# Optimization experiments

Hardware: AMD Instinct MI355X
Metric: run time of the kernel (lower is better)

## Reference

```python
import jax, jax.numpy as jnp
import numpy as np

B, I, D, H, DP = 2, 256, 768, 12, 128
DK = D // H  # 64
NPQ, NPV = 4, 8  # query/key points and value points per head


def setup_inputs() -> dict:
    key = jax.random.key(0)
    ks = jax.random.split(key, 24)
    s = 0.02
    w = lambda k, shp: (jax.random.normal(k, shp, jnp.float32) * s)
    inp = {
        "x1d": jax.random.normal(ks[0], (B, I, D), jnp.float32),
        "x2d": jax.random.normal(ks[1], (B, I, I, DP), jnp.float32),
        "past_T": jax.random.normal(ks[2], (B, I, 3), jnp.float32),
        "past_R": jax.random.normal(ks[3], (B, I, 3, 3), jnp.float32),
        "last_T": jax.random.normal(ks[4], (B, I, 3), jnp.float32),
        "last_R": jax.random.normal(ks[5], (B, I, 3, 3), jnp.float32),
        "bias": jax.random.normal(ks[6], (B, H, I, I), jnp.float32) * 0.1,
        "Wq": w(ks[7], (D, D)),
        "Wk": w(ks[8], (D, D)),
        "Wv": w(ks[9], (D, D)),
        "W_pair_bias": w(ks[10], (DP, H)),
        "Wpq_past": w(ks[11], (D, H * NPQ * 3)),
        "Wpk_past": w(ks[12], (D, H * NPQ * 3)),
        "Wpv_past": w(ks[13], (D, H * NPV * 3)),
        "Wpq_last": w(ks[14], (D, H * NPQ * 3)),
        "Wpk_last": w(ks[15], (D, H * NPQ * 3)),
        "Wpv_last": w(ks[16], (D, H * NPV * 3)),
        "tpw_past": jax.random.uniform(ks[17], (H,), jnp.float32),
        "tpw_last": jax.random.uniform(ks[18], (H,), jnp.float32),
        "W_pair_value": w(ks[19], (DP, D)),
        "W_out": w(ks[20], (2 * D + 2 * H * 8 * 4, D)),
        "b_out": jnp.zeros((D,), jnp.float32),
    }
    return inp


def reference(x1d, x2d, past_T, past_R, last_T, last_R, bias,
              Wq, Wk, Wv, W_pair_bias,
              Wpq_past, Wpk_past, Wpv_past,
              Wpq_last, Wpk_last, Wpv_last,
              tpw_past, tpw_last, W_pair_value, W_out, b_out):
    b, i, d = x1d.shape
    h = tpw_past.shape[0]
    dk = d // h
    scalar_w = 1.0 / np.sqrt(3.0 * dk)
    point_w = 1.0 / np.sqrt(3.0 * 4.0 * 9.0 / 2.0)
    pair_w = 1.0 / np.sqrt(3.0)

    # scalar attention
    q = (x1d @ Wq).reshape(b, i, h, dk)
    k = (x1d @ Wk).reshape(b, i, h, dk)
    v = (x1d @ Wv).reshape(b, i, h, dk)
    scalar_attn = jnp.einsum('bihc,bjhc->bhij', q * scalar_w, k)

    past_IR = jnp.swapaxes(past_R, -1, -2)
    last_IR = jnp.swapaxes(last_R, -1, -2)

    def affine(pts, T, IR):  # pts: [b,i,h,c,3]
        return jnp.einsum('bipq,bihcq->bihcp', IR, pts) + T[:, :, None, None, :]

    def point_branch(Wpq, Wpk, Wpv, T, IR, tpw):
        qp = (x1d @ Wpq).reshape(b, i, h, NPQ, 3)
        kp = (x1d @ Wpk).reshape(b, i, h, NPQ, 3)
        vp = (x1d @ Wpv).reshape(b, i, h, NPV, 3)
        qg, kg, vg = affine(qp, T, IR), affine(kp, T, IR), affine(vp, T, IR)
        # pairwise point distances: [b,i,j,h,NPQ]
        dist = jnp.linalg.norm(qg[:, :, None] - kg[:, None], axis=-1)
        pw = point_w * jax.nn.softplus(tpw)  # [h]
        attn = -0.5 * pw[:, None, None] * jnp.transpose(dist.sum(-1), (0, 3, 1, 2))
        return attn, vg

    pa_past, vg_past = point_branch(Wpq_past, Wpk_past, Wpv_past, past_T, past_IR, tpw_past)
    pa_last, vg_last = point_branch(Wpq_last, Wpk_last, Wpv_last, last_T, last_IR, tpw_last)

    pair_attn = pair_w * jnp.transpose(x2d @ W_pair_bias, (0, 3, 1, 2))  # bhij

    attn = jax.nn.softmax(scalar_attn + pa_past + pa_last + pair_attn + bias, axis=-1)

    out_scalar = jnp.einsum('bhij,bjhc->bihc', attn, v).reshape(b, i, d)
    og_past = jnp.einsum('bhij,bjhcp->bihcp', attn, vg_past)
    og_last = jnp.einsum('bhij,bjhcp->bihcp', attn, vg_last)

    # NOTE: the original module inverts BOTH branches with the PAST pose (faithful).
    def inv_past(og):
        return jnp.einsum('bipq,bihcq->bihcp', past_R, og - past_T[:, :, None, None, :])

    ol_past = inv_past(og_past)
    ol_last = inv_past(og_last)
    n_past = jnp.linalg.norm(ol_past, axis=-1).reshape(b, i, h * NPV)
    n_last = jnp.linalg.norm(ol_last, axis=-1).reshape(b, i, h * NPV)
    ol_past = ol_past.reshape(b, i, h * NPV * 3)
    ol_last = ol_last.reshape(b, i, h * NPV * 3)

    v_pair = (x2d @ W_pair_value).reshape(b, i, i, h, dk)
    out_pair = jnp.einsum('bhij,bijhc->bihc', attn, v_pair).reshape(b, i, d)

    feat = jnp.concatenate([out_pair, out_scalar, ol_past, n_past, ol_last, n_last], axis=-1)
    return feat @ W_out + b_out  # dropout is identity at eval
```

## Files before the change

kernel.cpp:

```cpp
#include <hip/hip_runtime.h>
#include <hip/hip_bf16.h>
#include <math.h>

#define BB 2
#define II 256
#define DD 768
#define HH 12
#define DPP 128
#define NPQ 4
#define NPV 8
#define FEAT_DIM 2304
#define NPACK 3456

#define OFF_QKVPTS ((size_t)0)
#define OFF_PBATTN ((size_t)1769472)
#define OFF_X1DB   ((size_t)3342336)
#define OFF_VT     OFF_X1DB
#define OFF_W1T    ((size_t)3538944)
#define OFF_ABF    OFF_W1T
#define OFF_W2T    ((size_t)4866048)
#define OFF_FEATB  ((size_t)5750784)
#define OFF_QPTS   ((size_t)6340608)
#define OFF_KPTS   ((size_t)6488064)
#define OFF_QKHM   ((size_t)6635520)
#define OFF_VGJT   ((size_t)7028736)
#define OFF_WPVT   ((size_t)7176192)

#define SCALAR_W 0.07216878364870323f
#define POINT_W  0.13608276348795434f
#define PAIR_W   0.57735026918962576f

typedef __attribute__((ext_vector_type(8))) short short8;
typedef __attribute__((ext_vector_type(4))) short short4v;
typedef __attribute__((ext_vector_type(4))) float f32x4;
typedef __attribute__((ext_vector_type(16))) float f32x16;

__device__ inline ushort f2bf(float f) {
  __hip_bfloat16 h = __float2bfloat16(f);
  return *reinterpret_cast<ushort*>(&h);
}
__device__ inline float bf2f(short u) {
  return __uint_as_float(((unsigned int)(unsigned short)u) << 16);
}

__global__ __launch_bounds__(256)
void convert_x_kernel(const float* __restrict__ src, ushort* __restrict__ dst, int n8) {
  const int idx = blockIdx.x * 256 + threadIdx.x;
  if (idx >= n8) return;
  const float4 f0 = reinterpret_cast<const float4*>(src)[idx * 2 + 0];
  const float4 f1 = reinterpret_cast<const float4*>(src)[idx * 2 + 1];
  short8 v;
  v[0] = (short)f2bf(f0.x); v[1] = (short)f2bf(f0.y);
  v[2] = (short)f2bf(f0.z); v[3] = (short)f2bf(f0.w);
  v[4] = (short)f2bf(f1.x); v[5] = (short)f2bf(f1.y);
  v[6] = (short)f2bf(f1.z); v[7] = (short)f2bf(f1.w);
  reinterpret_cast<short8*>(dst)[idx] = v;
}

struct TJob { const float* src; ushort* dst; int K, N, sStride, dStride; };
struct TJobs { TJob j[11]; };

__global__ __launch_bounds__(256)
void transpose_pack_kernel(TJobs jobs) {
  const TJob J = jobs.j[blockIdx.z];
  const int k0 = blockIdx.y * 32, n0 = blockIdx.x * 32;
  if (k0 >= J.K || n0 >= J.N) return;
  __shared__ float t[32][33];
  const int tid = threadIdx.x;
  const int c = tid & 31, r = tid >> 5;
#pragma unroll
  for (int u = 0; u < 4; ++u) {
    const int kk = r + u * 8;
    t[kk][c] = (n0 + c < J.N) ? J.src[(size_t)(k0 + kk) * J.sStride + n0 + c] : 0.f;
  }
  __syncthreads();
#pragma unroll
  for (int u = 0; u < 4; ++u) {
    const int n = n0 + r + u * 8;
    if (n < J.N) J.dst[(size_t)n * J.dStride + k0 + c] = f2bf(t[c][r + u * 8]);
  }
}

__global__ __launch_bounds__(256)
void mfma_gemm_kernel(const ushort* __restrict__ A, const ushort* __restrict__ Bt,
                      float* __restrict__ C, const float* __restrict__ bias,
                      ushort* __restrict__ Cb, ushort* __restrict__ Vt, int N, int K) {
  __shared__ short a_s[64 * 64];
  __shared__ short b_s[64 * 64];
  const int tid = threadIdx.x;
  const int lane = tid & 63;
  const int wave = tid >> 6;
  const int wm = wave >> 1, wn = wave & 1;
  const int m0 = blockIdx.x * 64, n0 = blockIdx.y * 64;
  const int lrow = tid >> 3, lch = tid & 7;
  const int l15 = lane & 15, l7 = lane & 7, kq = lane >> 4;
  f32x4 acc[2][2] = {};
  for (int kc = 0; kc < K; kc += 64) {
#pragma unroll
    for (int u = 0; u < 2; ++u) {
      const int r = lrow + u * 32;
      const short8 av = *reinterpret_cast<const short8*>(A  + (size_t)(m0 + r) * K + kc + lch * 8);
      const short8 bv = *reinterpret_cast<const short8*>(Bt + (size_t)(n0 + r) * K + kc + lch * 8);
      const int sc = ((lch ^ (r & 7)) << 3);
      *reinterpret_cast<short8*>(&a_s[r * 64 + sc]) = av;
      *reinterpret_cast<short8*>(&b_s[r * 64 + sc]) = bv;
    }
    __syncthreads();
#pragma unroll
    for (int kk = 0; kk < 64; kk += 32) {
      const int ch = (kk >> 3) + kq;
      const int cx = ((ch ^ l7) << 3);
      short8 af[2], bf[2];
      af[0] = *reinterpret_cast<const short8*>(&a_s[(wm * 32 +      l15) * 64 + cx]);
      af[1] = *reinterpret_cast<const short8*>(&a_s[(wm * 32 + 16 + l15) * 64 + cx]);
      bf[0] = *reinterpret_cast<const short8*>(&b_s[(wn * 32 +      l15) * 64 + cx]);
      bf[1] = *reinterpret_cast<const short8*>(&b_s[(wn * 32 + 16 + l15) * 64 + cx]);
#pragma unroll
      for (int mt = 0; mt < 2; ++mt)
#pragma unroll
        for (int nt = 0; nt < 2; ++nt)
          acc[mt][nt] = __builtin_amdgcn_mfma_f32_16x16x32_bf16(af[mt], bf[nt], acc[mt][nt], 0, 0, 0);
    }
    __syncthreads();
  }
#pragma unroll
  for (int mt = 0; mt < 2; ++mt) {
    const int r0 = m0 + wm * 32 + mt * 16 + kq * 4;
#pragma unroll
    for (int nt = 0; nt < 2; ++nt) {
      const int c = n0 + wn * 32 + nt * 16 + l15;
      const float bv = bias ? bias[c] : 0.f;
#pragma unroll
      for (int rr = 0; rr < 4; ++rr) {
        const float val = acc[mt][nt][rr] + bv;
        const int m = r0 + rr;
        if (!Cb) {
          C[(size_t)m * N + c] = val;
        } else if (c < 1536) {
          const int bb = m >> 8, ii = m & 255;
          const int plane = (c >= 768) ? 1 : 0;
          const int hh = (c & 767) >> 6, cc2 = c & 63;
          Cb[((((size_t)plane * BB + bb) * HH + hh) * II + ii) * 64 + cc2] = f2bf(val);
        } else if (c < 2304) {
          const int bb = m >> 8, ii = m & 255;
          Vt[((size_t)bb * DD + (c - 1536)) * II + ii] = f2bf(val);
        } else {
          C[(size_t)m * N + c] = val;
        }
      }
    }
  }
}

struct XfJob { const float* T; const float* R; float* dstf; ushort* dstb;
               int np; int sub; int srccol; int mode; };
struct XfJobs { XfJob j[6]; };

__global__ __launch_bounds__(256)
void transform_kernel(const float* __restrict__ qkvpts, XfJobs jobs) {
  const XfJob J = jobs.j[blockIdx.y];
  const int idx = blockIdx.x * 256 + threadIdx.x;
  if (J.mode == 1) {
    const int hn = HH * J.np;
    if (idx >= BB * II * hn) return;
    const int bi = idx / hn, rem = idx - bi * hn;
    const float* p = qkvpts + (size_t)bi * NPACK + J.srccol + rem * 3;
    const float p0 = p[0], p1 = p[1], p2 = p[2];
    const float* R = J.R + (size_t)bi * 9;
    const float* T = J.T + (size_t)bi * 3;
    const float o0 = R[0] * p0 + R[3] * p1 + R[6] * p2 + T[0];
    const float o1 = R[1] * p0 + R[4] * p1 + R[7] * p2 + T[1];
    const float o2 = R[2] * p0 + R[5] * p1 + R[8] * p2 + T[2];
    const int h = rem / J.np, n = rem - h * J.np;
    const int b = bi >> 8, i = bi & 255;
    float* d = J.dstf + ((size_t)(b * HH + h) * II + i) * 24 + J.sub + n * 3;
    d[0] = o0; d[1] = o1; d[2] = o2;
  } else {
    if (idx >= BB * HH * J.np * II) return;
    const int i = idx & 255;
    int r2 = idx >> 8;
    const int n = r2 % J.np; r2 /= J.np;
    const int h = r2 % HH;
    const int b = r2 / HH;
    const int bi = b * II + i;
    const float* p = qkvpts + (size_t)bi * NPACK + J.srccol + (h * J.np + n) * 3;
    const float p0 = p[0], p1 = p[1], p2 = p[2];
    const float* R = J.R + (size_t)bi * 9;
    const float* T = J.T + (size_t)bi * 3;
    const float o0 = R[0] * p0 + R[3] * p1 + R[6] * p2 + T[0];
    const float o1 = R[1] * p0 + R[4] * p1 + R[7] * p2 + T[1];
    const float o2 = R[2] * p0 + R[5] * p1 + R[8] * p2 + T[2];
    if (J.mode == 2) {
      const int col = J.sub + h * 24 + n * 3;
      ushort* d = J.dstb + ((size_t)b * 576 + col) * II + i;
      d[0] = f2bf(o0); d[II] = f2bf(o1); d[2 * II] = f2bf(o2);
    } else {
      float* d = J.dstf + ((size_t)(b * HH + h) * 24 + J.sub + n * 3) * II + i;
      d[0] = o0; d[II] = o1; d[2 * II] = o2;
    }
  }
}

__global__ __launch_bounds__(256)
void pairbias_kernel(const float* __restrict__ x2d, const float* __restrict__ Wpb,
                     const float* __restrict__ bias, ushort* __restrict__ pbattn) {
  __shared__ ushort wpbT_s[16 * 136];
  __shared__ ushort pb_s[128 * 18];
  const int tid = threadIdx.x;
  const int bi = blockIdx.x;
  const int half = blockIdx.y;
  const int b = bi >> 8, i = bi & 255;
  for (int u = tid; u < 2048; u += 256) {
    const int h = u >> 7, p = u & 127;
    wpbT_s[h * 136 + p] = (h < 12) ? f2bf(Wpb[p * 12 + h]) : (ushort)0;
  }
  __syncthreads();
  const int lane = tid & 63, w = tid >> 6;
  const int l15 = lane & 15, kq = lane >> 4;
  const float* xbase = x2d + ((size_t)bi * II + half * 128) * DPP;
#pragma unroll
  for (int mi = 0; mi < 2; ++mi) {
    const int mt = w + mi * 4;
    const int jl = mt * 16 + l15;
    const float* arow = xbase + (size_t)jl * DPP;
    f32x4 acc = {};
#pragma unroll
    for (int kk = 0; kk < 4; ++kk) {
      const float4 f0 = *reinterpret_cast<const float4*>(arow + kk * 32 + kq * 8);
      const float4 f1 = *reinterpret_cast<const float4*>(arow + kk * 32 + kq * 8 + 4);
      short8 af;
      af[0] = (short)f2bf(f0.x); af[1] = (short)f2bf(f0.y);
      af[2] = (short)f2bf(f0.z); af[3] = (short)f2bf(f0.w);
      af[4] = (short)f2bf(f1.x); af[5] = (short)f2bf(f1.y);
      af[6] = (short)f2bf(f1.z); af[7] = (short)f2bf(f1.w);
      const short8 bf = *reinterpret_cast<const short8*>(&wpbT_s[l15 * 136 + kk * 32 + kq * 8]);
      acc = __builtin_amdgcn_mfma_f32_16x16x32_bf16(af, bf, acc, 0, 0, 0);
    }
#pragma unroll
    for (int rr = 0; rr < 4; ++rr)
      pb_s[(mt * 16 + kq * 4 + rr) * 18 + l15] = f2bf(acc[rr]);
  }
  __syncthreads();
  if (tid < 192) {
    const int h = tid >> 4, jq = tid & 15;
    const int jl0 = jq * 8;
    const size_t base = (((size_t)(b * HH + h) * II + i) * II) + half * 128 + jl0;
    const float4 bv0 = *reinterpret_cast<const float4*>(bias + base);
    const float4 bv1 = *reinterpret_cast<const float4*>(bias + base + 4);
    const float bv[8] = {bv0.x, bv0.y, bv0.z, bv0.w, bv1.x, bv1.y, bv1.z, bv1.w};
    short8 o;
#pragma unroll
    for (int e = 0; e < 8; ++e)
      o[e] = (short)f2bf(PAIR_W * bf2f((short)pb_s[(jl0 + e) * 18 + h]) + bv[e]);
    *reinterpret_cast<short8*>(pbattn + base) = o;
  }
}

__global__ __launch_bounds__(256)
void attn_kernel(const ushort* __restrict__ qkhm,
                 const float* __restrict__ qpts, const float* __restrict__ kpts,
                 const float* __restrict__ tpw_past, const float* __restrict__ tpw_last,
                 const ushort* __restrict__ pbattn, ushort* __restrict__ abf) {
  __shared__ float qp_s[16 * 24];
  __shared__ float pb_s[16 * 260];
  __shared__ float red_s[2][16 * 4];
  __shared__ ushort a_lds[16 * 264];
  const int tid = threadIdx.x;
  const int lane = tid & 63;
  const int w = tid >> 6;
  const int i0 = blockIdx.x * 16;
  const int h = blockIdx.y;
  const int b = blockIdx.z;
  const size_t bh = (size_t)b * HH + h;
  if (tid < 96)
    reinterpret_cast<float4*>(qp_s)[tid] =
        reinterpret_cast<const float4*>(qpts + (bh * II + i0) * 24)[tid];
  {
    const ushort* src = pbattn + (bh * II + i0) * II;
    for (int u = tid; u < 512; u += 256) {
      const int r = u >> 5, c8 = u & 31;
      const short8 v = *reinterpret_cast<const short8*>(src + (size_t)r * II + c8 * 8);
      float* d = &pb_s[r * 260 + c8 * 8];
#pragma unroll
      for (int e = 0; e < 8; ++e) d[e] = bf2f(v[e]);
    }
  }
  __syncthreads();
  const int l15 = lane & 15, kq = lane >> 4;
  const ushort* qrow = qkhm + (((size_t)b * HH + h) * II + i0 + l15) * 64;
  const ushort* kplane = qkhm + (((size_t)(BB + b) * HH + h) * II) * 64;
  const short8 af0 = *reinterpret_cast<const short8*>(qrow + kq * 8);
  const short8 af1 = *reinterpret_cast<const short8*>(qrow + 32 + kq * 8);
  const float pwp = 0.5f * POINT_W * log1pf(expf(tpw_past[h]));
  const float pwl = 0.5f * POINT_W * log1pf(expf(tpw_last[h]));
  const float* kpt = kpts + bh * 6144;
  float lg[4][4];
#pragma unroll
  for (int jb = 0; jb < 4; ++jb) {
    const int j = w * 64 + jb * 16 + l15;
    const ushort* krow = kplane + (size_t)j * 64;
    f32x4 acc = {};
    acc = __builtin_amdgcn_mfma_f32_16x16x32_bf16(
        af0, *reinterpret_cast<const short8*>(krow + kq * 8), acc, 0, 0, 0);
    acc = __builtin_amdgcn_mfma_f32_16x16x32_bf16(
        af1, *reinterpret_cast<const short8*>(krow + 32 + kq * 8), acc, 0, 0, 0);
    float kg[24];
#pragma unroll
    for (int c = 0; c < 24; ++c) kg[c] = kpt[c * 256 + j];
#pragma unroll
    for (int rr = 0; rr < 4; ++rr) {
      const int il = kq * 4 + rr;
      const float* qg = &qp_s[il * 24];
      float dp = 0.f, dl = 0.f;
#pragma unroll
      for (int n = 0; n < 4; ++n) {
        float dx = qg[n * 3] - kg[n * 3], dy = qg[n * 3 + 1] - kg[n * 3 + 1],
              dz = qg[n * 3 + 2] - kg[n * 3 + 2];
        dp += sqrtf(dx * dx + dy * dy + dz * dz);
        dx = qg[12 + n * 3] - kg[12 + n * 3]; dy = qg[12 + n * 3 + 1] - kg[12 + n * 3 + 1];
        dz = qg[12 + n * 3 + 2] - kg[12 + n * 3 + 2];
        dl += sqrtf(dx * dx + dy * dy + dz * dz);
      }
      lg[jb][rr] = SCALAR_W * acc[rr] - pwp * dp - pwl * dl + pb_s[il * 260 + j];
    }
  }
#pragma unroll
  for (int rr = 0; rr < 4; ++rr) {
    float m = fmaxf(fmaxf(lg[0][rr], lg[1][rr]), fmaxf(lg[2][rr], lg[3][rr]));
    m = fmaxf(m, __shfl_xor(m, 1));
    m = fmaxf(m, __shfl_xor(m, 2));
    m = fmaxf(m, __shfl_xor(m, 4));
    m = fmaxf(m, __shfl_xor(m, 8));
    if (l15 == 0) red_s[0][(kq * 4 + rr) * 4 + w] = m;
  }
  __syncthreads();
#pragma unroll
  for (int rr = 0; rr < 4; ++rr) {
    const int il = kq * 4 + rr;
    const float* r = &red_s[0][il * 4];
    const float m = fmaxf(fmaxf(r[0], r[1]), fmaxf(r[2], r[3]));
    float s = 0.f;
#pragma unroll
    for (int jb = 0; jb < 4; ++jb) { lg[jb][rr] = __expf(lg[jb][rr] - m); s += lg[jb][rr]; }
    s += __shfl_xor(s, 1); s += __shfl_xor(s, 2);
    s += __shfl_xor(s, 4); s += __shfl_xor(s, 8);
    if (l15 == 0) red_s[1][il * 4 + w] = s;
  }
  __syncthreads();
#pragma unroll
  for (int rr = 0; rr < 4; ++rr) {
    const int il = kq * 4 + rr;
    const float* r = &red_s[1][il * 4];
    const float inv = 1.f / (r[0] + r[1] + r[2] + r[3]);
#pragma unroll
    for (int jb = 0; jb < 4; ++jb)
      a_lds[il * 264 + w * 64 + jb * 16 + l15] = f2bf(lg[jb][rr] * inv);
  }
  __syncthreads();
  ushort* ab = abf + (bh * II + i0) * II;
#pragma unroll
  for (int u = 0; u < 2; ++u) {
    const int idx = tid + u * 256;
    const int r = idx >> 5, cc = idx & 31;
    *reinterpret_cast<short8*>(ab + (size_t)r * II + cc * 8) =
        *reinterpret_cast<const short8*>(&a_lds[r * 264 + cc * 8]);
  }
}

__global__ __launch_bounds__(256)
void wpair_kernel(const float* __restrict__ x2d, const ushort* __restrict__ abf,
                  const ushort* __restrict__ wpvt, ushort* __restrict__ featb) {
  __shared__ ushort a_s[16 * 256];
  __shared__ ushort tb[64 * 136];
  __shared__ float t_s[16][128];
  const int tid = threadIdx.x;
  const int bi = blockIdx.x;
  const int b = bi >> 8, i = bi & 255;
#pragma unroll
  for (int u = 0; u < 2; ++u) {
    const int c = tid + u * 256;
    const int h = c >> 5, ch = c & 31;
    short8 v = {};
    if (h < 12)
      v = *reinterpret_cast<const short8*>(abf + (((size_t)(b * HH + h) * II + i) * II) + ch * 8);
    *reinterpret_cast<short8*>(&a_s[h * 256 + ((ch ^ h) << 3)]) = v;
  }
  const int lane = tid & 63, w = tid >> 6;
  const int l15 = lane & 15, kq = lane >> 4;
  const int n0 = w * 32;
  f32x4 acc[2] = {};
  for (int jt = 0; jt < 4; ++jt) {
    __syncthreads();
    const float4* src = reinterpret_cast<const float4*>(x2d + ((size_t)bi * II + jt * 64) * DPP);
#pragma unroll
    for (int u = 0; u < 8; ++u) {
      const int fid = tid + u * 256;
      const int j = fid >> 5, p4 = (fid & 31) * 4;
      const float4 v = src[fid];
      short4v o;
      o[0] = (short)f2bf(v.x); o[1] = (short)f2bf(v.y);
      o[2] = (short)f2bf(v.z); o[3] = (short)f2bf(v.w);
      *reinterpret_cast<short4v*>(&tb[j * 136 + (p4 ^ ((j >> 3) << 4))]) = o;
    }
    __syncthreads();
#pragma unroll
    for (int nt = 0; nt < 2; ++nt) {
      const int p = n0 + nt * 16 + l15;
#pragma unroll
      for (int kk = 0; kk < 2; ++kk) {
        const int ch32 = jt * 8 + kk * 4 + kq;
        const short8 af = *reinterpret_cast<const short8*>(&a_s[l15 * 256 + ((ch32 ^ l15) << 3)]);
        short8 bf;
#pragma unroll
        for (int e = 0; e < 8; ++e) {
          const int row = kk * 32 + kq * 8 + e;
          bf[e] = (short)tb[row * 136 + (p ^ ((row >> 3) << 4))];
        }
        acc[nt] = __builtin_amdgcn_mfma_f32_16x16x32_bf16(af, bf, acc[nt], 0, 0, 0);
      }
    }
  }
#pragma unroll
  for (int nt = 0; nt < 2; ++nt) {
    const int p = n0 + nt * 16 + l15;
#pragma unroll
    for (int r = 0; r < 4; ++r) t_s[kq * 4 + r][p] = acc[nt][r];
  }
  __syncthreads();
  ushort* fout = featb + (size_t)bi * FEAT_DIM;
#pragma unroll
  for (int u = 0; u < 3; ++u) {
    const int c = tid + u * 256;
    const int h = c >> 6;
    const ushort* wr = wpvt + (size_t)c * DPP;
    float o = 0.f;
    for (int p = 0; p < DPP; p += 8) {
      const short8 wv = *reinterpret_cast<const short8*>(wr + p);
#pragma unroll
      for (int e = 0; e < 8; ++e) o += t_s[h][p + e] * bf2f(wv[e]);
    }
    fout[c] = f2bf(o);
  }
}

__global__ __launch_bounds__(256)
void av_kernel(const ushort* __restrict__ abf, const ushort* __restrict__ vt,
               const ushort* __restrict__ vgjt,
               const float* __restrict__ past_T, const float* __restrict__ past_R,
               ushort* __restrict__ featb) {
  __shared__ ushort a_s[32 * 256];
  __shared__ float c_s[32][116];
  const int tid = threadIdx.x;
  const int it = blockIdx.x;
  const int h  = blockIdx.y;
  const int b  = blockIdx.z;
  const int i0 = it * 32;
  const size_t bh = (size_t)b * HH + h;
  {
    const ushort* src = abf + (bh * II + i0) * II;
#pragma unroll
    for (int u = 0; u < 4; ++u) {
      const int cidx = tid + u * 256;
      const int r = cidx >> 5, ch = cidx & 31;
      const short8 v = *reinterpret_cast<const short8*>(src + (size_t)r * II + ch * 8);
      *reinterpret_cast<short8*>(&a_s[r * 256 + ((ch ^ (r & 7)) << 3)]) = v;
    }
  }
  __syncthreads();
  const int lane = tid & 63, w = tid >> 6;
  const int l15 = lane & 15, kq = lane >> 4;
  for (int t = w; t < 14; t += 4) {
    const int mt = t / 7, nt = t % 7;
    const int c = nt * 16 + l15;
    const ushort* bcol;
    if (c < 64)      bcol = vt   + ((size_t)b * DD + h * 64 + c) * II;
    else if (c < 88) bcol = vgjt + ((size_t)b * 576 + h * 24 + (c - 64)) * II;
    else             bcol = vgjt + ((size_t)b * 576 + 288 + h * 24 + (c - 88)) * II;
    f32x4 acc = {};
#pragma unroll
    for (int ks = 0; ks < 8; ++ks) {
      const int ch = ks * 4 + kq;
      const int r = mt * 16 + l15;
      const short8 af = *reinterpret_cast<const short8*>(&a_s[r * 256 + ((ch ^ (r & 7)) << 3)]);
      const short8 bf = *reinterpret_cast<const short8*>(bcol + ks * 32 + kq * 8);
      acc = __builtin_amdgcn_mfma_f32_16x16x32_bf16(af, bf, acc, 0, 0, 0);
    }
#pragma unroll
    for (int rr = 0; rr < 4; ++rr) c_s[mt * 16 + kq * 4 + rr][c] = acc[rr];
  }
  __syncthreads();
  {
    const int il = tid >> 3, c0 = (tid & 7) * 8;
    ushort* fo = featb + (size_t)(b * II + i0 + il) * FEAT_DIM + 768 + h * 64 + c0;
    short8 o;
#pragma unroll
    for (int e = 0; e < 8; ++e) o[e] = (short)f2bf(c_s[il][c0 + e]);
    *reinterpret_cast<short8*>(fo) = o;
  }
  for (int u = tid; u < 512; u += 256) {
    const int il = u >> 4;
    const int br = (u >> 3) & 1;
    const int n = u & 7;
    const int bi = b * II + i0 + il;
    const float* T = past_T + (size_t)bi * 3;
    const float* R = past_R + (size_t)bi * 9;
    const int cb = 64 + br * 24 + n * 3;
    const float o0 = c_s[il][cb + 0] - T[0];
    const float o1 = c_s[il][cb + 1] - T[1];
    const float o2 = c_s[il][cb + 2] - T[2];
    const float l0 = R[0] * o0 + R[1] * o1 + R[2] * o2;
    const float l1 = R[3] * o0 + R[4] * o1 + R[5] * o2;
    const float l2 = R[6] * o0 + R[7] * o1 + R[8] * o2;
    const float nn = sqrtf(l0 * l0 + l1 * l1 + l2 * l2);
    const int r = h * 8 + n;
    ushort* fout = featb + (size_t)bi * FEAT_DIM;
    const int olbase = br ? 1920 : 1536;
    const int nbase  = br ? 2208 : 1824;
    fout[olbase + r * 3 + 0] = f2bf(l0);
    fout[olbase + r * 3 + 1] = f2bf(l1);
    fout[olbase + r * 3 + 2] = f2bf(l2);
    fout[nbase + r] = f2bf(nn);
  }
}

extern "C" void kernel_launch(void* const* d_in, const int* in_sizes, int n_in,
                              void* d_out, int out_size, void* d_ws, size_t ws_size,
                              hipStream_t stream) {
  (void)in_sizes; (void)n_in; (void)out_size; (void)ws_size;
  const float* x1d      = (const float*)d_in[0];
  const float* x2d      = (const float*)d_in[1];
  const float* past_T   = (const float*)d_in[2];
  const float* past_R   = (const float*)d_in[3];
  const float* last_T   = (const float*)d_in[4];
  const float* last_R   = (const float*)d_in[5];
  const float* bias     = (const float*)d_in[6];
  const float* Wq       = (const float*)d_in[7];
  const float* Wk       = (const float*)d_in[8];
  const float* Wv       = (const float*)d_in[9];
  const float* Wpb      = (const float*)d_in[10];
  const float* Wpq_past = (const float*)d_in[11];
  const float* Wpk_past = (const float*)d_in[12];
  const float* Wpv_past = (const float*)d_in[13];
  const float* Wpq_last = (const float*)d_in[14];
  const float* Wpk_last = (const float*)d_in[15];
  const float* Wpv_last = (const float*)d_in[16];
  const float* tpw_past = (const float*)d_in[17];
  const float* tpw_last = (const float*)d_in[18];
  const float* W_pair_value = (const float*)d_in[19];
  const float* W_out    = (const float*)d_in[20];
  const float* b_out    = (const float*)d_in[21];
  float* out = (float*)d_out;
  float* ws  = (float*)d_ws;

  float*  qkvpts = ws + OFF_QKVPTS;
  ushort* pbattn = (ushort*)(ws + OFF_PBATTN);
  ushort* x1db   = (ushort*)(ws + OFF_X1DB);
  ushort* vt     = (ushort*)(ws + OFF_VT);
  ushort* w1t    = (ushort*)(ws + OFF_W1T);
  ushort* abf    = (ushort*)(ws + OFF_ABF);
  ushort* w2t    = (ushort*)(ws + OFF_W2T);
  ushort* featb  = (ushort*)(ws + OFF_FEATB);
  float*  qpts   = ws + OFF_QPTS;
  float*  kpts   = ws + OFF_KPTS;
  ushort* qkhm   = (ushort*)(ws + OFF_QKHM);
  ushort* vgjt   = (ushort*)(ws + OFF_VGJT);
  ushort* wpvt   = (ushort*)(ws + OFF_WPVT);

  const dim3 blk256(256);

  pairbias_kernel<<<dim3(BB * II, 2), blk256, 0, stream>>>(x2d, Wpb, bias, pbattn);

  convert_x_kernel<<<dim3(192), blk256, 0, stream>>>(x1d, x1db, 512 * 768 / 8);

  {
    TJobs jobs = {};
    jobs.j[0]  = {Wq,       w1t + (size_t)   0 * 768, DD,      DD,   DD,  768};
    jobs.j[1]  = {Wk,       w1t + (size_t) 768 * 768, DD,      DD,   DD,  768};
    jobs.j[2]  = {Wv,       w1t + (size_t)1536 * 768, DD,      DD,   DD,  768};
    jobs.j[3]  = {Wpq_past, w1t + (size_t)2304 * 768, DD,     144,   144, 768};
    jobs.j[4]  = {Wpk_past, w1t + (size_t)2448 * 768, DD,     144,   144, 768};
    jobs.j[5]  = {Wpv_past, w1t + (size_t)2592 * 768, DD,     288,   288, 768};
    jobs.j[6]  = {Wpq_last, w1t + (size_t)2880 * 768, DD,     144,   144, 768};
    jobs.j[7]  = {Wpk_last, w1t + (size_t)3024 * 768, DD,     144,   144, 768};
    jobs.j[8]  = {Wpv_last, w1t + (size_t)3168 * 768, DD,     288,   288, 768};
    jobs.j[9]  = {W_out,    w2t,                      FEAT_DIM, DD,  DD,  2304};
    jobs.j[10] = {W_pair_value, wpvt,                 DPP,     DD,   DD,  DPP};
    transpose_pack_kernel<<<dim3(24, 72, 11), blk256, 0, stream>>>(jobs);
  }

  mfma_gemm_kernel<<<dim3(8, 54), blk256, 0, stream>>>(
      x1db, w1t, qkvpts, nullptr, qkhm, vt, NPACK, DD);

  {
    XfJobs jobs = {};
    jobs.j[0] = {past_T, past_R, qpts, nullptr, NPQ,   0, 2304, 1};
    jobs.j[1] = {past_T, past_R, kpts, nullptr, NPQ,   0, 2448, 3};
    jobs.j[2] = {past_T, past_R, nullptr, vgjt, NPV,   0, 2592, 2};
    jobs.j[3] = {last_T, last_R, qpts, nullptr, NPQ,  12, 2880, 1};
    jobs.j[4] = {last_T, last_R, kpts, nullptr, NPQ,  12, 3024, 3};
    jobs.j[5] = {last_T, last_R, nullptr, vgjt, NPV, 288, 3168, 2};
    transform_kernel<<<dim3(192, 6), blk256, 0, stream>>>(qkvpts, jobs);
  }

  attn_kernel<<<dim3(16, HH, BB), blk256, 0, stream>>>(
      qkhm, qpts, kpts, tpw_past, tpw_last, pbattn, abf);

  wpair_kernel<<<dim3(BB * II), blk256, 0, stream>>>(x2d, abf, wpvt, featb);

  av_kernel<<<dim3(8, HH, BB), blk256, 0, stream>>>(
      abf, vt, vgjt, past_T, past_R, featb);

  mfma_gemm_kernel<<<dim3(8, 12), blk256, 0, stream>>>(
      featb, w2t, out, b_out, nullptr, nullptr, DD, FEAT_DIM);
}
```

Baseline: 125.3 us.

## Merge prep kernels and wpair/av kernels into block-dispatched launches

```diff
diff --git a/kernel.cpp b/kernel.cpp
--- a/kernel.cpp
+++ b/kernel.cpp
@@ -33,7 +33,6 @@
 typedef __attribute__((ext_vector_type(8))) short short8;
 typedef __attribute__((ext_vector_type(4))) short short4v;
 typedef __attribute__((ext_vector_type(4))) float f32x4;
-typedef __attribute__((ext_vector_type(16))) float f32x16;
 
 __device__ inline ushort f2bf(float f) {
   __hip_bfloat16 h = __float2bfloat16(f);
@@ -43,41 +42,103 @@
   return __uint_as_float(((unsigned int)(unsigned short)u) << 16);
 }
 
+struct TJob { const float* src; ushort* dst; int K, N, sStride, dStride, nx, ny; };
+struct TJobs { TJob j[11]; };
+
 __global__ __launch_bounds__(256)
-void convert_x_kernel(const float* __restrict__ src, ushort* __restrict__ dst, int n8) {
-  const int idx = blockIdx.x * 256 + threadIdx.x;
-  if (idx >= n8) return;
-  const float4 f0 = reinterpret_cast<const float4*>(src)[idx * 2 + 0];
-  const float4 f1 = reinterpret_cast<const float4*>(src)[idx * 2 + 1];
-  short8 v;
-  v[0] = (short)f2bf(f0.x); v[1] = (short)f2bf(f0.y);
-  v[2] = (short)f2bf(f0.z); v[3] = (short)f2bf(f0.w);
-  v[4] = (short)f2bf(f1.x); v[5] = (short)f2bf(f1.y);
-  v[6] = (short)f2bf(f1.z); v[7] = (short)f2bf(f1.w);
-  reinterpret_cast<short8*>(dst)[idx] = v;
-}
-
-struct TJob { const float* src; ushort* dst; int K, N, sStride, dStride; };
-struct TJobs { TJob j[11]; };
-
-__global__ __launch_bounds__(256)
-void transpose_pack_kernel(TJobs jobs) {
-  const TJob J = jobs.j[blockIdx.z];
-  const int k0 = blockIdx.y * 32, n0 = blockIdx.x * 32;
-  if (k0 >= J.K || n0 >= J.N) return;
-  __shared__ float t[32][33];
+void prep_kernel(const float* __restrict__ x2d, const float* __restrict__ Wpb,
+                 const float* __restrict__ bias, ushort* __restrict__ pbattn,
+                 const float* __restrict__ x1d, ushort* __restrict__ x1db,
+                 TJobs jobs) {
+  __shared__ __align__(16) char smem[9216];
+  const int blk = blockIdx.x;
   const int tid = threadIdx.x;
-  const int c = tid & 31, r = tid >> 5;
-#pragma unroll
-  for (int u = 0; u < 4; ++u) {
-    const int kk = r + u * 8;
-    t[kk][c] = (n0 + c < J.N) ? J.src[(size_t)(k0 + kk) * J.sStride + n0 + c] : 0.f;
-  }
-  __syncthreads();
-#pragma unroll
-  for (int u = 0; u < 4; ++u) {
-    const int n = n0 + r + u * 8;
-    if (n < J.N) J.dst[(size_t)n * J.dStride + k0 + c] = f2bf(t[c][r + u * 8]);
+  if (blk < 1024) {
+    ushort* wpbT_s = (ushort*)smem;
+    ushort* pb_s   = (ushort*)(smem + 4352);
+    const int bi = blk >> 1, half = blk & 1;
+    const int b = bi >> 8, i = bi & 255;
+    for (int u = tid; u < 2048; u += 256) {
+      const int h = u >> 7, p = u & 127;
+      wpbT_s[h * 136 + p] = (h < 12) ? f2bf(Wpb[p * 12 + h]) : (ushort)0;
+    }
+    __syncthreads();
+    const int lane = tid & 63, w = tid >> 6;
+    const int l15 = lane & 15, kq = lane >> 4;
+    const float* xbase = x2d + ((size_t)bi * II + half * 128) * DPP;
+#pragma unroll
+    for (int mi = 0; mi < 2; ++mi) {
+      const int mt = w + mi * 4;
+      const int jl = mt * 16 + l15;
+      const float* arow = xbase + (size_t)jl * DPP;
+      f32x4 acc = {};
+#pragma unroll
+      for (int kk = 0; kk < 4; ++kk) {
+        const float4 f0 = *reinterpret_cast<const float4*>(arow + kk * 32 + kq * 8);
+        const float4 f1 = *reinterpret_cast<const float4*>(arow + kk * 32 + kq * 8 + 4);
+        short8 af;
+        af[0] = (short)f2bf(f0.x); af[1] = (short)f2bf(f0.y);
+        af[2] = (short)f2bf(f0.z); af[3] = (short)f2bf(f0.w);
+        af[4] = (short)f2bf(f1.x); af[5] = (short)f2bf(f1.y);
+        af[6] = (short)f2bf(f1.z); af[7] = (short)f2bf(f1.w);
+        const short8 bf = *reinterpret_cast<const short8*>(&wpbT_s[l15 * 136 + kk * 32 + kq * 8]);
+        acc = __builtin_amdgcn_mfma_f32_16x16x32_bf16(af, bf, acc, 0, 0, 0);
+      }
+#pragma unroll
+      for (int rr = 0; rr < 4; ++rr)
+        pb_s[(mt * 16 + kq * 4 + rr) * 18 + l15] = f2bf(acc[rr]);
+    }
+    __syncthreads();
+    if (tid < 192) {
+      const int h = tid >> 4, jq = tid & 15;
+      const int jl0 = jq * 8;
+      const size_t base = (((size_t)(b * HH + h) * II + i) * II) + half * 128 + jl0;
+      const float4 bv0 = *reinterpret_cast<const float4*>(bias + base);
+      const float4 bv1 = *reinterpret_cast<const float4*>(bias + base + 4);
+      const float bv[8] = {bv0.x, bv0.y, bv0.z, bv0.w, bv1.x, bv1.y, bv1.z, bv1.w};
+      short8 o;
+#pragma unroll
+      for (int e = 0; e < 8; ++e)
+        o[e] = (short)f2bf(PAIR_W * bf2f((short)pb_s[(jl0 + e) * 18 + h]) + bv[e]);
+      *reinterpret_cast<short8*>(pbattn + base) = o;
+    }
+  } else if (blk < 1216) {
+    const int idx = (blk - 1024) * 256 + tid;
+    if (idx < 512 * 768 / 8) {
+      const float4 f0 = reinterpret_cast<const float4*>(x1d)[idx * 2 + 0];
+      const float4 f1 = reinterpret_cast<const float4*>(x1d)[idx * 2 + 1];
+      short8 v;
+      v[0] = (short)f2bf(f0.x); v[1] = (short)f2bf(f0.y);
+      v[2] = (short)f2bf(f0.z); v[3] = (short)f2bf(f0.w);
+      v[4] = (short)f2bf(f1.x); v[5] = (short)f2bf(f1.y);
+      v[6] = (short)f2bf(f1.z); v[7] = (short)f2bf(f1.w);
+      reinterpret_cast<short8*>(x1db)[idx] = v;
+    }
+  } else {
+    float (*t)[33] = (float(*)[33])smem;
+    int blk2 = blk - 1216;
+#pragma unroll 1
+    for (int jj = 0; jj < 11; ++jj) {
+      const TJob J = jobs.j[jj];
+      const int cnt = J.nx * J.ny;
+      if (blk2 < cnt) {
+        const int n0 = (blk2 % J.nx) * 32, k0 = (blk2 / J.nx) * 32;
+        const int c = tid & 31, r = tid >> 5;
+#pragma unroll
+        for (int u = 0; u < 4; ++u) {
+          const int kk = r + u * 8;
+          t[kk][c] = (n0 + c < J.N) ? J.src[(size_t)(k0 + kk) * J.sStride + n0 + c] : 0.f;
+        }
+        __syncthreads();
+#pragma unroll
+        for (int u = 0; u < 4; ++u) {
+          const int n = n0 + r + u * 8;
+          if (n < J.N) J.dst[(size_t)n * J.dStride + k0 + c] = f2bf(t[c][r + u * 8]);
+        }
+        return;
+      }
+      blk2 -= cnt;
+    }
   }
 }
 
@@ -202,61 +263,6 @@
 }
 
 __global__ __launch_bounds__(256)
-void pairbias_kernel(const float* __restrict__ x2d, const float* __restrict__ Wpb,
-                     const float* __restrict__ bias, ushort* __restrict__ pbattn) {
-  __shared__ ushort wpbT_s[16 * 136];
-  __shared__ ushort pb_s[128 * 18];
-  const int tid = threadIdx.x;
-  const int bi = blockIdx.x;
-  const int half = blockIdx.y;
-  const int b = bi >> 8, i = bi & 255;
-  for (int u = tid; u < 2048; u += 256) {
-    const int h = u >> 7, p = u & 127;
-    wpbT_s[h * 136 + p] = (h < 12) ? f2bf(Wpb[p * 12 + h]) : (ushort)0;
-  }
-  __syncthreads();
-  const int lane = tid & 63, w = tid >> 6;
-  const int l15 = lane & 15, kq = lane >> 4;
-  const float* xbase = x2d + ((size_t)bi * II + half * 128) * DPP;
-#pragma unroll
-  for (int mi = 0; mi < 2; ++mi) {
-    const int mt = w + mi * 4;
-    const int jl = mt * 16 + l15;
-    const float* arow = xbase + (size_t)jl * DPP;
-    f32x4 acc = {};
-#pragma unroll
-    for (int kk = 0; kk < 4; ++kk) {
-      const float4 f0 = *reinterpret_cast<const float4*>(arow + kk * 32 + kq * 8);
-      const float4 f1 = *reinterpret_cast<const float4*>(arow + kk * 32 + kq * 8 + 4);
-      short8 af;
-      af[0] = (short)f2bf(f0.x); af[1] = (short)f2bf(f0.y);
-      af[2] = (short)f2bf(f0.z); af[3] = (short)f2bf(f0.w);
-      af[4] = (short)f2bf(f1.x); af[5] = (short)f2bf(f1.y);
-      af[6] = (short)f2bf(f1.z); af[7] = (short)f2bf(f1.w);
-      const short8 bf = *reinterpret_cast<const short8*>(&wpbT_s[l15 * 136 + kk * 32 + kq * 8]);
-      acc = __builtin_amdgcn_mfma_f32_16x16x32_bf16(af, bf, acc, 0, 0, 0);
-    }
-#pragma unroll
-    for (int rr = 0; rr < 4; ++rr)
-      pb_s[(mt * 16 + kq * 4 + rr) * 18 + l15] = f2bf(acc[rr]);
-  }
-  __syncthreads();
-  if (tid < 192) {
-    const int h = tid >> 4, jq = tid & 15;
-    const int jl0 = jq * 8;
-    const size_t base = (((size_t)(b * HH + h) * II + i) * II) + half * 128 + jl0;
-    const float4 bv0 = *reinterpret_cast<const float4*>(bias + base);
-    const float4 bv1 = *reinterpret_cast<const float4*>(bias + base + 4);
-    const float bv[8] = {bv0.x, bv0.y, bv0.z, bv0.w, bv1.x, bv1.y, bv1.z, bv1.w};
-    short8 o;
-#pragma unroll
-    for (int e = 0; e < 8; ++e)
-      o[e] = (short)f2bf(PAIR_W * bf2f((short)pb_s[(jl0 + e) * 18 + h]) + bv[e]);
-    *reinterpret_cast<short8*>(pbattn + base) = o;
-  }
-}
-
-__global__ __launch_bounds__(256)
 void attn_kernel(const ushort* __restrict__ qkhm,
                  const float* __restrict__ qpts, const float* __restrict__ kpts,
                  const float* __restrict__ tpw_past, const float* __restrict__ tpw_last,
@@ -368,158 +374,158 @@
 }
 
 __global__ __launch_bounds__(256)
-void wpair_kernel(const float* __restrict__ x2d, const ushort* __restrict__ abf,
-                  const ushort* __restrict__ wpvt, ushort* __restrict__ featb) {
-  __shared__ ushort a_s[16 * 256];
-  __shared__ ushort tb[64 * 136];
-  __shared__ float t_s[16][128];
+void wpair_av_kernel(const float* __restrict__ x2d, const ushort* __restrict__ abf,
+                     const ushort* __restrict__ wpvt,
+                     const ushort* __restrict__ vt, const ushort* __restrict__ vgjt,
+                     const float* __restrict__ past_T, const float* __restrict__ past_R,
+                     ushort* __restrict__ featb) {
+  __shared__ __align__(16) char smem[33792];
+  const int blk = blockIdx.x;
   const int tid = threadIdx.x;
-  const int bi = blockIdx.x;
-  const int b = bi >> 8, i = bi & 255;
-#pragma unroll
-  for (int u = 0; u < 2; ++u) {
-    const int c = tid + u * 256;
-    const int h = c >> 5, ch = c & 31;
-    short8 v = {};
-    if (h < 12)
-      v = *reinterpret_cast<const short8*>(abf + (((size_t)(b * HH + h) * II + i) * II) + ch * 8);
-    *reinterpret_cast<short8*>(&a_s[h * 256 + ((ch ^ h) << 3)]) = v;
-  }
   const int lane = tid & 63, w = tid >> 6;
   const int l15 = lane & 15, kq = lane >> 4;
-  const int n0 = w * 32;
-  f32x4 acc[2] = {};
-  for (int jt = 0; jt < 4; ++jt) {
-    __syncthreads();
-    const float4* src = reinterpret_cast<const float4*>(x2d + ((size_t)bi * II + jt * 64) * DPP);
-#pragma unroll
-    for (int u = 0; u < 8; ++u) {
-      const int fid = tid + u * 256;
-      const int j = fid >> 5, p4 = (fid & 31) * 4;
-      const float4 v = src[fid];
-      short4v o;
-      o[0] = (short)f2bf(v.x); o[1] = (short)f2bf(v.y);
-      o[2] = (short)f2bf(v.z); o[3] = (short)f2bf(v.w);
-      *reinterpret_cast<short4v*>(&tb[j * 136 + (p4 ^ ((j >> 3) << 4))]) = o;
-    }
-    __syncthreads();
+  if (blk < 512) {
+    ushort* a_s = (ushort*)smem;
+    ushort* tb  = (ushort*)(smem + 8192);
+    float*  t_s = (float*)(smem + 25600);
+    const int bi = blk;
+    const int b = bi >> 8, i = bi & 255;
+#pragma unroll
+    for (int u = 0; u < 2; ++u) {
+      const int c = tid + u * 256;
+      const int h = c >> 5, ch = c & 31;
+      short8 v = {};
+      if (h < 12)
+        v = *reinterpret_cast<const short8*>(abf + (((size_t)(b * HH + h) * II + i) * II) + ch * 8);
+      *reinterpret_cast<short8*>(&a_s[h * 256 + ((ch ^ h) << 3)]) = v;
+    }
+    const int n0 = w * 32;
+    f32x4 acc[2] = {};
+    for (int jt = 0; jt < 4; ++jt) {
+      __syncthreads();
+      const float4* src = reinterpret_cast<const float4*>(x2d + ((size_t)bi * II + jt * 64) * DPP);
+#pragma unroll
+      for (int u = 0; u < 8; ++u) {
+        const int fid = tid + u * 256;
+        const int j = fid >> 5, p4 = (fid & 31) * 4;
+        const float4 v = src[fid];
+        short4v o;
+        o[0] = (short)f2bf(v.x); o[1] = (short)f2bf(v.y);
+        o[2] = (short)f2bf(v.z); o[3] = (short)f2bf(v.w);
+        *reinterpret_cast<short4v*>(&tb[j * 136 + (p4 ^ ((j >> 3) << 4))]) = o;
+      }
+      __syncthreads();
+#pragma unroll
+      for (int nt = 0; nt < 2; ++nt) {
+        const int p = n0 + nt * 16 + l15;
+#pragma unroll
+        for (int kk = 0; kk < 2; ++kk) {
+          const int ch32 = jt * 8 + kk * 4 + kq;
+          const short8 af = *reinterpret_cast<const short8*>(&a_s[l15 * 256 + ((ch32 ^ l15) << 3)]);
+          short8 bf;
+#pragma unroll
+          for (int e = 0; e < 8; ++e) {
+            const int row = kk * 32 + kq * 8 + e;
+            bf[e] = (short)tb[row * 136 + (p ^ ((row >> 3) << 4))];
+          }
+          acc[nt] = __builtin_amdgcn_mfma_f32_16x16x32_bf16(af, bf, acc[nt], 0, 0, 0);
+        }
+      }
+    }
 #pragma unroll
     for (int nt = 0; nt < 2; ++nt) {
       const int p = n0 + nt * 16 + l15;
 #pragma unroll
-      for (int kk = 0; kk < 2; ++kk) {
-        const int ch32 = jt * 8 + kk * 4 + kq;
-        const short8 af = *reinterpret_cast<const short8*>(&a_s[l15 * 256 + ((ch32 ^ l15) << 3)]);
-        short8 bf;
-#pragma unroll
-        for (int e = 0; e < 8; ++e) {
-          const int row = kk * 32 + kq * 8 + e;
-          bf[e] = (short)tb[row * 136 + (p ^ ((row >> 3) << 4))];
-        }
-        acc[nt] = __builtin_amdgcn_mfma_f32_16x16x32_bf16(af, bf, acc[nt], 0, 0, 0);
-      }
-    }
-  }
-#pragma unroll
-  for (int nt = 0; nt < 2; ++nt) {
-    const int p = n0 + nt * 16 + l15;
-#pragma unroll
-    for (int r = 0; r < 4; ++r) t_s[kq * 4 + r][p] = acc[nt][r];
-  }
-  __syncthreads();
-  ushort* fout = featb + (size_t)bi * FEAT_DIM;
-#pragma unroll
-  for (int u = 0; u < 3; ++u) {
-    const int c = tid + u * 256;
-    const int h = c >> 6;
-    const ushort* wr = wpvt + (size_t)c * DPP;
-    float o = 0.f;
-    for (int p = 0; p < DPP; p += 8) {
-      const short8 wv = *reinterpret_cast<const short8*>(wr + p);
-#pragma unroll
-      for (int e = 0; e < 8; ++e) o += t_s[h][p + e] * bf2f(wv[e]);
-    }
-    fout[c] = f2bf(o);
-  }
-}
-
-__global__ __launch_bounds__(256)
-void av_kernel(const ushort* __restrict__ abf, const ushort* __restrict__ vt,
-               const ushort* __restrict__ vgjt,
-               const float* __restrict__ past_T, const float* __restrict__ past_R,
-               ushort* __restrict__ featb) {
-  __shared__ ushort a_s[32 * 256];
-  __shared__ float c_s[32][116];
-  const int tid = threadIdx.x;
-  const int it = blockIdx.x;
-  const int h  = blockIdx.y;
-  const int b  = blockIdx.z;
-  const int i0 = it * 32;
-  const size_t bh = (size_t)b * HH + h;
-  {
-    const ushort* src = abf + (bh * II + i0) * II;
-#pragma unroll
-    for (int u = 0; u < 4; ++u) {
-      const int cidx = tid + u * 256;
-      const int r = cidx >> 5, ch = cidx & 31;
-      const short8 v = *reinterpret_cast<const short8*>(src + (size_t)r * II + ch * 8);
-      *reinterpret_cast<short8*>(&a_s[r * 256 + ((ch ^ (r & 7)) << 3)]) = v;
-    }
-  }
-  __syncthreads();
-  const int lane = tid & 63, w = tid >> 6;
-  const int l15 = lane & 15, kq = lane >> 4;
-  for (int t = w; t < 14; t += 4) {
-    const int mt = t / 7, nt = t % 7;
-    const int c = nt * 16 + l15;
-    const ushort* bcol;
-    if (c < 64)      bcol = vt   + ((size_t)b * DD + h * 64 + c) * II;
-    else if (c < 88) bcol = vgjt + ((size_t)b * 576 + h * 24 + (c - 64)) * II;
-    else             bcol = vgjt + ((size_t)b * 576 + 288 + h * 24 + (c - 88)) * II;
-    f32x4 acc = {};
-#pragma unroll
-    for (int ks = 0; ks < 8; ++ks) {
-      const int ch = ks * 4 + kq;
-      const int r = mt * 16 + l15;
-      const short8 af = *reinterpret_cast<const short8*>(&a_s[r * 256 + ((ch ^ (r & 7)) << 3)]);
-      const short8 bf = *reinterpret_cast<const short8*>(bcol + ks * 32 + kq * 8);
-      acc = __builtin_amdgcn_mfma_f32_16x16x32_bf16(af, bf, acc, 0, 0, 0);
-    }
-#pragma unroll
-    for (int rr = 0; rr < 4; ++rr) c_s[mt * 16 + kq * 4 + rr][c] = acc[rr];
-  }
-  __syncthreads();
-  {
-    const int il = tid >> 3, c0 = (tid & 7) * 8;
-    ushort* fo = featb + (size_t)(b * II + i0 + il) * FEAT_DIM + 768 + h * 64 + c0;
-    short8 o;
-#pragma unroll
-    for (int e = 0; e < 8; ++e) o[e] = (short)f2bf(c_s[il][c0 + e]);
-    *reinterpret_cast<short8*>(fo) = o;
-  }
-  for (int u = tid; u < 512; u += 256) {
-    const int il = u >> 4;
-    const int br = (u >> 3) & 1;
-    const int n = u & 7;
-    const int bi = b * II + i0 + il;
-    const float* T = past_T + (size_t)bi * 3;
-    const float* R = past_R + (size_t)bi * 9;
-    const int cb = 64 + br * 24 + n * 3;
-    const float o0 = c_s[il][cb + 0] - T[0];
-    const float o1 = c_s[il][cb + 1] - T[1];
-    const float o2 = c_s[il][cb + 2] - T[2];
-    const float l0 = R[0] * o0 + R[1] * o1 + R[2] * o2;
-    const float l1 = R[3] * o0 + R[4] * o1 + R[5] * o2;
-    const float l2 = R[6] * o0 + R[7] * o1 + R[8] * o2;
-    const float nn = sqrtf(l0 * l0 + l1 * l1 + l2 * l2);
-    const int r = h * 8 + n;
+      for (int r = 0; r < 4; ++r) t_s[(kq * 4 + r) * 128 + p] = acc[nt][r];
+    }
+    __syncthreads();
     ushort* fout = featb + (size_t)bi * FEAT_DIM;
-    const int olbase = br ? 1920 : 1536;
-    const int nbase  = br ? 2208 : 1824;
-    fout[olbase + r * 3 + 0] = f2bf(l0);
-    fout[olbase + r * 3 + 1] = f2bf(l1);
-    fout[olbase + r * 3 + 2] = f2bf(l2);
-    fout[nbase + r] = f2bf(nn);
+#pragma unroll
+    for (int u = 0; u < 3; ++u) {
+      const int c = tid + u * 256;
+      const int h = c >> 6;
+      const ushort* wr = wpvt + (size_t)c * DPP;
+      float o = 0.f;
+      for (int p = 0; p < DPP; p += 8) {
+        const short8 wv = *reinterpret_cast<const short8*>(wr + p);
+#pragma unroll
+        for (int e = 0; e < 8; ++e) o += t_s[h * 128 + p + e] * bf2f(wv[e]);
+      }
+      fout[c] = f2bf(o);
+    }
+  } else {
+    ushort* a_s = (ushort*)smem;
+    float*  c_s = (float*)(smem + 16384);
+    const int blk2 = blk - 512;
+    const int it = blk2 & 7;
+    const int rest = blk2 >> 3;
+    const int h = rest % 12;
+    const int b = rest / 12;
+    const int i0 = it * 32;
+    const size_t bh = (size_t)b * HH + h;
+    {
+      const ushort* src = abf + (bh * II + i0) * II;
+#pragma unroll
+      for (int u = 0; u < 4; ++u) {
+        const int cidx = tid + u * 256;
+        const int r = cidx >> 5, ch = cidx & 31;
+        const short8 v = *reinterpret_cast<const short8*>(src + (size_t)r * II + ch * 8);
+        *reinterpret_cast<short8*>(&a_s[r * 256 + ((ch ^ (r & 7)) << 3)]) = v;
+      }
+    }
+    __syncthreads();
+    for (int t = w; t < 14; t += 4) {
+      const int mt = t / 7, nt = t % 7;
+      const int c = nt * 16 + l15;
+      const ushort* bcol;
+      if (c < 64)      bcol = vt   + ((size_t)b * DD + h * 64 + c) * II;
+      else if (c < 88) bcol = vgjt + ((size_t)b * 576 + h * 24 + (c - 64)) * II;
+      else             bcol = vgjt + ((size_t)b * 576 + 288 + h * 24 + (c - 88)) * II;
+      f32x4 acc = {};
+#pragma unroll
+      for (int ks = 0; ks < 8; ++ks) {
+        const int ch = ks * 4 + kq;
+        const int r = mt * 16 + l15;
+        const short8 af = *reinterpret_cast<const short8*>(&a_s[r * 256 + ((ch ^ (r & 7)) << 3)]);
+        const short8 bf = *reinterpret_cast<const short8*>(bcol + ks * 32 + kq * 8);
+        acc = __builtin_amdgcn_mfma_f32_16x16x32_bf16(af, bf, acc, 0, 0, 0);
+      }
+#pragma unroll
+      for (int rr = 0; rr < 4; ++rr) c_s[(mt * 16 + kq * 4 + rr) * 116 + c] = acc[rr];
+    }
+    __syncthreads();
+    {
+      const int il = tid >> 3, c0 = (tid & 7) * 8;
+      ushort* fo = featb + (size_t)(b * II + i0 + il) * FEAT_DIM + 768 + h * 64 + c0;
+      short8 o;
+#pragma unroll
+      for (int e = 0; e < 8; ++e) o[e] = (short)f2bf(c_s[il * 116 + c0 + e]);
+      *reinterpret_cast<short8*>(fo) = o;
+    }
+    for (int u = tid; u < 512; u += 256) {
+      const int il = u >> 4;
+      const int br = (u >> 3) & 1;
+      const int n = u & 7;
+      const int bi = b * II + i0 + il;
+      const float* T = past_T + (size_t)bi * 3;
+      const float* R = past_R + (size_t)bi * 9;
+      const int cb = 64 + br * 24 + n * 3;
+      const float o0 = c_s[il * 116 + cb + 0] - T[0];
+      const float o1 = c_s[il * 116 + cb + 1] - T[1];
+      const float o2 = c_s[il * 116 + cb + 2] - T[2];
+      const float l0 = R[0] * o0 + R[1] * o1 + R[2] * o2;
+      const float l1 = R[3] * o0 + R[4] * o1 + R[5] * o2;
+      const float l2 = R[6] * o0 + R[7] * o1 + R[8] * o2;
+      const float nn = sqrtf(l0 * l0 + l1 * l1 + l2 * l2);
+      const int r = h * 8 + n;
+      ushort* fout = featb + (size_t)bi * FEAT_DIM;
+      const int olbase = br ? 1920 : 1536;
+      const int nbase  = br ? 2208 : 1824;
+      fout[olbase + r * 3 + 0] = f2bf(l0);
+      fout[olbase + r * 3 + 1] = f2bf(l1);
+      fout[olbase + r * 3 + 2] = f2bf(l2);
+      fout[nbase + r] = f2bf(nn);
+    }
   }
 }
 
@@ -568,24 +574,23 @@
 
   const dim3 blk256(256);
 
-  pairbias_kernel<<<dim3(BB * II, 2), blk256, 0, stream>>>(x2d, Wpb, bias, pbattn);
-
-  convert_x_kernel<<<dim3(192), blk256, 0, stream>>>(x1d, x1db, 512 * 768 / 8);
-
   {
     TJobs jobs = {};
-    jobs.j[0]  = {Wq,       w1t + (size_t)   0 * 768, DD,      DD,   DD,  768};
-    jobs.j[1]  = {Wk,       w1t + (size_t) 768 * 768, DD,      DD,   DD,  768};
-    jobs.j[2]  = {Wv,       w1t + (size_t)1536 * 768, DD,      DD,   DD,  768};
-    jobs.j[3]  = {Wpq_past, w1t + (size_t)2304 * 768, DD,     144,   144, 768};
-    jobs.j[4]  = {Wpk_past, w1t + (size_t)2448 * 768, DD,     144,   144, 768};
-    jobs.j[5]  = {Wpv_past, w1t + (size_t)2592 * 768, DD,     288,   288, 768};
-    jobs.j[6]  = {Wpq_last, w1t + (size_t)2880 * 768, DD,     144,   144, 768};
-    jobs.j[7]  = {Wpk_last, w1t + (size_t)3024 * 768, DD,     144,   144, 768};
-    jobs.j[8]  = {Wpv_last, w1t + (size_t)3168 * 768, DD,     288,   288, 768};
-    jobs.j[9]  = {W_out,    w2t,                      FEAT_DIM, DD,  DD,  2304};
-    jobs.j[10] = {W_pair_value, wpvt,                 DPP,     DD,   DD,  DPP};
-    transpose_pack_kernel<<<dim3(24, 72, 11), blk256, 0, stream>>>(jobs);
+    jobs.j[0]  = {Wq,       w1t + (size_t)   0 * 768, DD,      DD,   DD,  768,  24, 24};
+    jobs.j[1]  = {Wk,       w1t + (size_t) 768 * 768, DD,      DD,   DD,  768,  24, 24};
+    jobs.j[2]  = {Wv,       w1t + (size_t)1536 * 768, DD,      DD,   DD,  768,  24, 24};
+    jobs.j[3]  = {Wpq_past, w1t + (size_t)2304 * 768, DD,     144,   144, 768,   5, 24};
+    jobs.j[4]  = {Wpk_past, w1t + (size_t)2448 * 768, DD,     144,   144, 768,   5, 24};
+    jobs.j[5]  = {Wpv_past, w1t + (size_t)2592 * 768, DD,     288,   288, 768,   9, 24};
+    jobs.j[6]  = {Wpq_last, w1t + (size_t)2880 * 768, DD,     144,   144, 768,   5, 24};
+    jobs.j[7]  = {Wpk_last, w1t + (size_t)3024 * 768, DD,     144,   144, 768,   5, 24};
+    jobs.j[8]  = {Wpv_last, w1t + (size_t)3168 * 768, DD,     288,   288, 768,   9, 24};
+    jobs.j[9]  = {W_out,    w2t,                      FEAT_DIM, DD,  DD,  2304, 24, 72};
+    jobs.j[10] = {W_pair_value, wpvt,                 DPP,     DD,   DD,  DPP,  24,  4};
+    int tblocks = 0;
+    for (int j = 0; j < 11; ++j) tblocks += jobs.j[j].nx * jobs.j[j].ny;
+    prep_kernel<<<dim3(1216 + tblocks), blk256, 0, stream>>>(
+        x2d, Wpb, bias, pbattn, x1d, x1db, jobs);
   }
 
   mfma_gemm_kernel<<<dim3(8, 54), blk256, 0, stream>>>(
@@ -605,10 +610,8 @@
   attn_kernel<<<dim3(16, HH, BB), blk256, 0, stream>>>(
       qkhm, qpts, kpts, tpw_past, tpw_last, pbattn, abf);
 
-  wpair_kernel<<<dim3(BB * II), blk256, 0, stream>>>(x2d, abf, wpvt, featb);
-
-  av_kernel<<<dim3(8, HH, BB), blk256, 0, stream>>>(
-      abf, vt, vgjt, past_T, past_R, featb);
+  wpair_av_kernel<<<dim3(704), blk256, 0, stream>>>(
+      x2d, abf, wpvt, vt, vgjt, past_T, past_R, featb);
 
   mfma_gemm_kernel<<<dim3(8, 12), blk256, 0, stream>>>(
       featb, w2t, out, b_out, nullptr, nullptr, DD, FEAT_DIM);
```

Result: faster. 115.3 us, median of 2 (-8.0%).
